# Kernel tuning notes

Hardware: AMD Instinct MI355X
Metric: run time of the kernel (lower is better)

Reference implementation:

```python
import jax, jax.numpy as jnp
import numpy as np

H, D = 16, 64  # num_attention_heads, attention_head_size
BASE = 10000.0

def _rope(q, k, seq_len):
    # RotaryPositionalEmbedding: inv_freq over arange(0, D, 2); emb = cat(freqs, freqs)
    inv_freq = 1.0 / (BASE ** (jnp.arange(0, D, 2, dtype=jnp.float32) / D))  # [D/2]=32
    pos = jnp.arange(seq_len, dtype=jnp.float32)
    freqs = jnp.outer(pos, inv_freq)            # [S, 32]; equals cos_emb[..., :d]
    cos, sin = jnp.cos(freqs), jnp.sin(freqs)   # [S, 32]
    d = D // 2                                   # 32: only first half of head dim rotated
    half = d // 2                                # 16: internal rotate-half within rot part
    def rot(x):  # x: [B, H, S, D]
        xr, xp = x[..., :d], x[..., d:]
        swapped = jnp.concatenate([xr[..., half:], xr[..., :half]], axis=-1)
        xr2 = xr * cos - swapped * sin
        return jnp.concatenate([xr2, xp], axis=-1)
    return rot(q), rot(k)

def setup_inputs() -> dict:
    key = jax.random.key(0)
    ks = jax.random.split(key, 9)
    B, S, E = 2, 2048, 1024
    std = 0.02  # initializer_range
    inp = {"hidden_states": jax.random.normal(ks[0], (B, S, E), jnp.float32)}
    for i, n in enumerate(["q", "k", "v", "d"]):
        inp[f"W{n}"] = jax.random.normal(ks[1 + 2 * i], (E, E), jnp.float32) * std
        inp[f"b{n}"] = jnp.zeros((E,), jnp.float32)
    return inp

def reference(hidden_states, Wq, bq, Wk, bk, Wv, bv, Wd, bd):
    B, S, E = hidden_states.shape
    def heads(x):  # [B,S,E] -> [B,H,S,D]
        return x.reshape(B, S, H, D).transpose(0, 2, 1, 3)
    q = heads(hidden_states @ Wq + bq)
    k = heads(hidden_states @ Wk + bk)
    v = heads(hidden_states @ Wv + bv)
    q, k = _rope(q, k, S)
    scores = jnp.einsum("bhqd,bhkd->bhqk", q, k) / jnp.sqrt(jnp.float32(D))
    causal = jnp.tril(jnp.ones((S, S), dtype=bool))
    scores = jnp.where(causal, scores, -jnp.inf)
    probs = jax.nn.softmax(scores, axis=-1)
    ctx = jnp.einsum("bhqk,bhkd->bhqd", probs, v)
    ctx = ctx.transpose(0, 2, 1, 3).reshape(B, S, E)
    return ctx @ Wd + bd
```

## Files before the change

kernel.cpp:

```cpp
#include <hip/hip_runtime.h>
#include <stdint.h>

typedef __bf16 bf8 __attribute__((ext_vector_type(8)));
typedef float f4 __attribute__((ext_vector_type(4)));
typedef float f16v __attribute__((ext_vector_type(16)));
typedef unsigned short us8 __attribute__((ext_vector_type(8)));
typedef unsigned short us4 __attribute__((ext_vector_type(4)));

#define MFMA16(a, b, c) __builtin_amdgcn_mfma_f32_16x16x32_bf16(a, b, c, 0, 0, 0)
#define MFMA32(a, b, c) __builtin_amdgcn_mfma_f32_32x32x16_bf16(a, b, c, 0, 0, 0)

__device__ __forceinline__ unsigned short f2b(float f) {
  union { float f; unsigned u; } x; x.f = f;
  unsigned u = x.u;
  u += 0x7fffu + ((u >> 16) & 1u);
  return (unsigned short)(u >> 16);
}

__device__ __forceinline__ unsigned cvtpk(float a, float b) {
  unsigned r;
  asm("v_cvt_pk_bf16_f32 %0, %1, %2" : "=v"(r) : "v"(a), "v"(b));
  return r;
}

__device__ __forceinline__ void plswap(unsigned &a, unsigned &b) {
  asm("v_permlane32_swap_b32 %0, %1" : "+v"(a), "+v"(b));
}

__device__ __forceinline__ void gload16(const void* g, void* l) {
  __builtin_amdgcn_global_load_lds(
      (const __attribute__((address_space(1))) void*)g,
      (__attribute__((address_space(3))) void*)l, 16, 0, 0);
}

__global__ __launch_bounds__(256) void prep_kernel(
    const float* __restrict__ W0, const float* __restrict__ W1,
    const float* __restrict__ W2, const float* __restrict__ W3,
    unsigned short* __restrict__ T0, unsigned short* __restrict__ T1,
    unsigned short* __restrict__ T2, unsigned short* __restrict__ T3,
    const float* __restrict__ hid, unsigned short* __restrict__ hb) {
  if (blockIdx.z == 4) {
    int bi = blockIdx.x + 32 * blockIdx.y;
#pragma unroll
    for (int k = 0; k < 4; ++k) {
      int i = bi * 1024 + k * 256 + threadIdx.x;
      float4 v = ((const float4*)hid)[i];
      us4 r = { f2b(v.x), f2b(v.y), f2b(v.z), f2b(v.w) };
      *(us4*)(hb + (size_t)i * 4) = r;
    }
    return;
  }
  const float* W; unsigned short* Wt;
  if (blockIdx.z == 0)      { W = W0; Wt = T0; }
  else if (blockIdx.z == 1) { W = W1; Wt = T1; }
  else if (blockIdx.z == 2) { W = W2; Wt = T2; }
  else                      { W = W3; Wt = T3; }
  __shared__ float tile[32][33];
  int tx = threadIdx.x & 31, ty = threadIdx.x >> 5;
  int kb = blockIdx.x * 32, nb = blockIdx.y * 32;
#pragma unroll
  for (int j = 0; j < 32; j += 8)
    tile[ty + j][tx] = W[(size_t)(kb + ty + j) * 1024 + nb + tx];
  __syncthreads();
#pragma unroll
  for (int j = 0; j < 32; j += 8)
    Wt[(size_t)(nb + ty + j) * 1024 + kb + tx] = f2b(tile[tx][ty + j]);
}

__global__ __launch_bounds__(256) void gemm_qkv_kernel(
    const unsigned short* __restrict__ X,
    const unsigned short* __restrict__ Wqt, const unsigned short* __restrict__ Wkt,
    const unsigned short* __restrict__ Wvt,
    const float* __restrict__ bq, const float* __restrict__ bk,
    const float* __restrict__ bv,
    unsigned short* __restrict__ Qo, unsigned short* __restrict__ Ko,
    unsigned short* __restrict__ Vo) {
  const unsigned short* Wt; const float* bias; unsigned short* out;
  if (blockIdx.z == 0)      { Wt = Wqt; bias = bq; out = Qo; }
  else if (blockIdx.z == 1) { Wt = Wkt; bias = bk; out = Ko; }
  else                      { Wt = Wvt; bias = bv; out = Vo; }

  __shared__ __align__(16) unsigned short shmem[128 * 136];
  unsigned short* As = shmem;
  unsigned short* Bs = shmem + 128 * 64;
  const int t = threadIdx.x;
  const int wave = t >> 6, lane = t & 63, quad = lane >> 4, l16 = lane & 15;
  const int wm = (wave >> 1) * 64, wn = (wave & 1) * 64;
  const int L = blockIdx.x + 8 * blockIdx.y;
  const int xcd = L & 7, w = L >> 3;
  const int m0 = (xcd * 4 + (w >> 3)) * 128;
  const int n0 = (w & 7) * 128;

  f4 acc[4][4];
#pragma unroll
  for (int mi = 0; mi < 4; ++mi)
#pragma unroll
    for (int ni = 0; ni < 4; ++ni) acc[mi][ni] = (f4)0.0f;

  for (int k0 = 0; k0 < 1024; k0 += 64) {
    __syncthreads();
#pragma unroll
    for (int it = 0; it < 4; ++it) {
      int chunk = it * 256 + wave * 64 + lane;
      int row = chunk >> 3, cc = chunk & 7;
      int csw = cc ^ (row & 7);
      gload16(&X[(size_t)(m0 + row) * 1024 + k0 + csw * 8],
              &As[(size_t)(it * 256 + wave * 64) * 8]);
      gload16(&Wt[(size_t)(n0 + row) * 1024 + k0 + csw * 8],
              &Bs[(size_t)(it * 256 + wave * 64) * 8]);
    }
    __syncthreads();
#pragma unroll
    for (int kk = 0; kk < 2; ++kk) {
      const int sw = (kk * 4 + quad) ^ (l16 & 7);
      bf8 a[4], b[4];
#pragma unroll
      for (int mi = 0; mi < 4; ++mi)
        a[mi] = *(const bf8*)&As[(wm + mi * 16 + l16) * 64 + sw * 8];
#pragma unroll
      for (int ni = 0; ni < 4; ++ni)
        b[ni] = *(const bf8*)&Bs[(wn + ni * 16 + l16) * 64 + sw * 8];
#pragma unroll
      for (int mi = 0; mi < 4; ++mi)
#pragma unroll
        for (int ni = 0; ni < 4; ++ni)
          acc[mi][ni] = MFMA16(a[mi], b[ni], acc[mi][ni]);
    }
  }

  float biasv[4];
#pragma unroll
  for (int ni = 0; ni < 4; ++ni) biasv[ni] = bias[n0 + wn + ni * 16 + l16];

  if (blockIdx.z < 2) {
    const float kr = 13.287712379549449f / 32.0f;
    const float f0 = exp2f(-(float)l16 * kr);
    const float f1 = exp2f(-(float)(l16 + 16) * kr);
    const float qs = (blockIdx.z == 0) ? 0.18033688011112042f : 1.0f;
#pragma unroll
    for (int mi = 0; mi < 4; ++mi) {
#pragma unroll
      for (int r = 0; r < 4; ++r) {
        int m = m0 + wm + mi * 16 + quad * 4 + r;
        float s = (float)(m & 2047);
        float s0, c0, s1, c1;
        __sincosf(s * f0, &s0, &c0);
        __sincosf(s * f1, &s1, &c1);
        float v0 = acc[mi][0][r] + biasv[0];
        float v1 = acc[mi][1][r] + biasv[1];
        acc[mi][0][r] = (v0 * c0 - v1 * s0) * qs;
        acc[mi][1][r] = (v1 * c1 - v0 * s1) * qs;
        acc[mi][2][r] = (acc[mi][2][r] + biasv[2]) * qs;
        acc[mi][3][r] = (acc[mi][3][r] + biasv[3]) * qs;
      }
    }
    __syncthreads();
#pragma unroll
    for (int ni = 0; ni < 4; ++ni)
#pragma unroll
      for (int mi = 0; mi < 4; ++mi)
#pragma unroll
        for (int r = 0; r < 4; ++r)
          shmem[(wm + mi * 16 + quad * 4 + r) * 136 + wn + ni * 16 + l16] =
              f2b(acc[mi][ni][r]);
    __syncthreads();
    const int b_ = m0 >> 11;
    const int sBase = m0 & 2047;
    if (blockIdx.z == 0) {
#pragma unroll
      for (int it = 0; it < 8; ++it) {
        int p = wave * 8 + it;
        int s3 = p >> 1, hloc = p & 1;
        int row = s3 * 8 + (lane >> 3);
        us8 v = *(const us8*)&shmem[row * 136 + hloc * 64 + (lane & 7) * 8];
        int h = (n0 >> 6) + hloc;
        *(us8*)&out[((size_t)(((b_ << 4) | h) * 2048 + sBase + row)) * 64 +
                    (lane & 7) * 8] = v;
      }
    } else {
#pragma unroll
      for (int it = 0; it < 8; ++it) {
        int p = wave * 8 + it;
        int s5 = p >> 3, hloc = (p >> 2) & 1, c4 = p & 3;
        int row = s5 * 32 + (lane & 31);
        int hl_ = lane >> 5;
        us8 v = *(const us8*)&shmem[row * 136 + hloc * 64 + c4 * 16 + hl_ * 8];
        int h = (n0 >> 6) + hloc;
        size_t off = (size_t)((b_ << 4) | h) * 131072
                   + (size_t)((sBase >> 5) + s5) * 2048 + (lane & 31) * 8
                   + c4 * 512 + hl_ * 256;
        *(us8*)&out[off] = v;
      }
    }
  } else {
#pragma unroll
    for (int ni = 0; ni < 4; ++ni) {
      int n = n0 + wn + ni * 16 + l16;
      int h = n >> 6, d = n & 63;
      int dpart = ((d >> 5) & 1) * 2048 + (d & 31) * 8;
#pragma unroll
      for (int mi = 0; mi < 4; ++mi) {
        int m = m0 + wm + mi * 16 + quad * 4;
        int b_ = m >> 11, s = m & 2047;
        us4 w2 = { f2b(acc[mi][ni][0] + biasv[ni]), f2b(acc[mi][ni][1] + biasv[ni]),
                   f2b(acc[mi][ni][2] + biasv[ni]), f2b(acc[mi][ni][3] + biasv[ni]) };
        size_t off = (size_t)((b_ << 4) | h) * 131072
                   + (size_t)(s >> 6) * 4096 + ((s >> 4) & 3) * 512
                   + ((s >> 3) & 1) * 256 + dpart + (s & 7);
        *(us4*)&out[off] = w2;
      }
    }
  }
}

__global__ __launch_bounds__(256) void flash_attn_kernel(
    const unsigned short* __restrict__ Q, const unsigned short* __restrict__ K,
    const unsigned short* __restrict__ Vt, unsigned short* __restrict__ ctx) {
  __shared__ __align__(16) float osh[2][64][36];
  __shared__ float lsh[2][64];
  const int t = threadIdx.x;
  const int lane = t & 63;
  const int wave = t >> 6, l32 = lane & 31, hl = lane >> 5;
  const int sub = wave >> 1;
  const int kh  = wave & 1;

  const int id = blockIdx.x;
  const int bh = id & 31;
  const int j = id >> 5;
  const int qt = (j & 16) ? (31 - (j & 15)) : (j & 15);
  const int b = bh >> 4, h = bh & 15;

  const unsigned short* Qh = Q + (size_t)bh * 131072;
  const unsigned short* Kh = K + (size_t)bh * 131072;
  const unsigned short* Vh = Vt + (size_t)bh * 131072;

  const int wrow0 = qt * 64 + sub * 32;
  const int q = wrow0 + l32;

  bf8 qb[4];
#pragma unroll
  for (int c = 0; c < 4; ++c)
    qb[c] = *(const bf8*)&Qh[(size_t)q * 64 + c * 16 + hl * 8];

  f16v o0 = (f16v)0.0f, o1 = (f16v)0.0f;
  float sum = 0.0f;

  bf8 kfA[2][4], kfB[2][4];
  const int nk = qt + 1;
  const int kb = kh ? (nk >> 1) : 0;
  const int ke = kh ? nk : (nk >> 1);

  auto loadK = [&](bf8 (&kf)[2][4], int kt) {
    const unsigned short* p = Kh + (size_t)kt * 4096 + lane * 8;
#pragma unroll
    for (int mt = 0; mt < 2; ++mt)
#pragma unroll
      for (int c = 0; c < 4; ++c)
        kf[mt][c] = *(const bf8*)&p[mt * 2048 + c * 512];
  };

  auto step = [&](int kt, bf8 (&kf)[2][4]) {
    const int k0 = kt * 64;

    f16v s0 = (f16v)0.0f, s1 = (f16v)0.0f;
#pragma unroll
    for (int c = 0; c < 4; ++c) {
      s0 = MFMA32(kf[0][c], qb[c], s0);
      s1 = MFMA32(kf[1][c], qb[c], s1);
    }
    __builtin_amdgcn_sched_barrier(0);

    const unsigned short* pv = Vh + (size_t)kt * 4096 + lane * 8;
    bf8 vf[2][4];
#pragma unroll
    for (int c = 0; c < 4; ++c)
#pragma unroll
      for (int dt = 0; dt < 2; ++dt)
        vf[dt][c] = *(const bf8*)&pv[dt * 2048 + c * 512];

    if (kt == nk - 1) {
#pragma unroll
      for (int gg = 0; gg < 4; ++gg)
#pragma unroll
        for (int i = 0; i < 4; ++i) {
          int kk = k0 + gg * 8 + hl * 4 + i;
          if (kk > q) s0[gg * 4 + i] = -3e38f;
          if (kk + 32 > q) s1[gg * 4 + i] = -3e38f;
        }
    }

    {
      uint2 pd2[4];
#pragma unroll
      for (int gg = 0; gg < 4; ++gg) {
        float p0 = exp2f(s0[gg * 4 + 0]), p1 = exp2f(s0[gg * 4 + 1]);
        float p2 = exp2f(s0[gg * 4 + 2]), p3 = exp2f(s0[gg * 4 + 3]);
        sum += (p0 + p1) + (p2 + p3);
        pd2[gg].x = cvtpk(p0, p1); pd2[gg].y = cvtpk(p2, p3);
      }
#pragma unroll
      for (int c = 0; c < 2; ++c) {
        unsigned ax = pd2[2 * c].x, bx = pd2[2 * c + 1].x;
        unsigned ay = pd2[2 * c].y, by = pd2[2 * c + 1].y;
        plswap(ax, bx);
        plswap(ay, by);
        union { uint4 u; bf8 v; } pv2; pv2.u = (uint4){ax, ay, bx, by};
        o0 = MFMA32(vf[0][c], pv2.v, o0);
        o1 = MFMA32(vf[1][c], pv2.v, o1);
      }
    }
    {
      uint2 pd2[4];
#pragma unroll
      for (int gg = 0; gg < 4; ++gg) {
        float r0 = exp2f(s1[gg * 4 + 0]), r1 = exp2f(s1[gg * 4 + 1]);
        float r2 = exp2f(s1[gg * 4 + 2]), r3 = exp2f(s1[gg * 4 + 3]);
        sum += (r0 + r1) + (r2 + r3);
        pd2[gg].x = cvtpk(r0, r1); pd2[gg].y = cvtpk(r2, r3);
      }
#pragma unroll
      for (int c = 0; c < 2; ++c) {
        unsigned ax = pd2[2 * c].x, bx = pd2[2 * c + 1].x;
        unsigned ay = pd2[2 * c].y, by = pd2[2 * c + 1].y;
        plswap(ax, bx);
        plswap(ay, by);
        union { uint4 u; bf8 v; } pv2; pv2.u = (uint4){ax, ay, bx, by};
        o0 = MFMA32(vf[0][2 + c], pv2.v, o0);
        o1 = MFMA32(vf[1][2 + c], pv2.v, o1);
      }
    }
  };

  if (kb < ke) {
    loadK(kfA, kb);
    int kt = kb;
    while (true) {
      if (kt + 1 < ke) loadK(kfB, kt + 1);
      step(kt, kfA);
      ++kt; if (kt >= ke) break;
      if (kt + 1 < ke) loadK(kfA, kt + 1);
      step(kt, kfB);
      ++kt; if (kt >= ke) break;
    }
  }

  float lpart = sum + __shfl_xor(sum, 32);

  if (kh == 0) {
#pragma unroll
    for (int gg = 0; gg < 4; ++gg) {
      f4 w0 = { o0[gg * 4 + 0], o0[gg * 4 + 1], o0[gg * 4 + 2], o0[gg * 4 + 3] };
      *(f4*)&osh[sub][lane][gg * 4] = w0;
      f4 w1 = { o1[gg * 4 + 0], o1[gg * 4 + 1], o1[gg * 4 + 2], o1[gg * 4 + 3] };
      *(f4*)&osh[sub][lane][16 + gg * 4] = w1;
    }
    lsh[sub][lane] = lpart;
  }
  __syncthreads();
  if (kh == 1) {
    float inv = 1.0f / (lpart + lsh[sub][lane]);
#pragma unroll
    for (int gg = 0; gg < 4; ++gg) {
      int d0 = gg * 8 + hl * 4;
      f4 a0 = *(f4*)&osh[sub][lane][gg * 4];
      f4 a1 = *(f4*)&osh[sub][lane][16 + gg * 4];
      us4 w0 = { f2b((o0[gg * 4 + 0] + a0[0]) * inv), f2b((o0[gg * 4 + 1] + a0[1]) * inv),
                 f2b((o0[gg * 4 + 2] + a0[2]) * inv), f2b((o0[gg * 4 + 3] + a0[3]) * inv) };
      *(us4*)&ctx[((size_t)(b * 2048 + q)) * 1024 + h * 64 + d0] = w0;
      us4 w1 = { f2b((o1[gg * 4 + 0] + a1[0]) * inv), f2b((o1[gg * 4 + 1] + a1[1]) * inv),
                 f2b((o1[gg * 4 + 2] + a1[2]) * inv), f2b((o1[gg * 4 + 3] + a1[3]) * inv) };
      *(us4*)&ctx[((size_t)(b * 2048 + q)) * 1024 + h * 64 + 32 + d0] = w1;
    }
  }
}

__global__ __launch_bounds__(256) void gemm_out_kernel(
    const unsigned short* __restrict__ A,
    const unsigned short* __restrict__ Wt,
    const float* __restrict__ bias, float* __restrict__ out) {
  __shared__ unsigned short As[64 * 64];
  __shared__ unsigned short Bs[128 * 64];
  const int t = threadIdx.x;
  const int wave = t >> 6, lane = t & 63, quad = lane >> 4, l16 = lane & 15;
  const int wm = (wave & 1) * 32, wn = (wave >> 1) * 64;
  const int L = blockIdx.x + 8 * blockIdx.y;
  const int xcd = L & 7, w = L >> 3;
  const int m0 = (xcd * 8 + (w >> 3)) * 64;
  const int n0 = (w & 7) * 128;

  f4 acc[2][4];
#pragma unroll
  for (int mi = 0; mi < 2; ++mi)
#pragma unroll
    for (int ni = 0; ni < 4; ++ni) acc[mi][ni] = (f4)0.0f;

  for (int k0 = 0; k0 < 1024; k0 += 64) {
    __syncthreads();
    {
#pragma unroll
      for (int it = 0; it < 2; ++it) {
        int chunk = it * 256 + wave * 64 + lane;
        int row = chunk >> 3, cc = chunk & 7;
        gload16(&A[(size_t)(m0 + row) * 1024 + k0 + (cc ^ (row & 7)) * 8],
                &As[(size_t)(it * 256 + wave * 64) * 8]);
      }
#pragma unroll
      for (int it = 0; it < 4; ++it) {
        int chunk = it * 256 + wave * 64 + lane;
        int row = chunk >> 3, cc = chunk & 7;
        gload16(&Wt[(size_t)(n0 + row) * 1024 + k0 + (cc ^ (row & 7)) * 8],
                &Bs[(size_t)(it * 256 + wave * 64) * 8]);
      }
    }
    __syncthreads();
#pragma unroll
    for (int kk = 0; kk < 2; ++kk) {
      const int sw = (kk * 4 + quad) ^ (l16 & 7);
      bf8 a[2], b[4];
#pragma unroll
      for (int mi = 0; mi < 2; ++mi)
        a[mi] = *(const bf8*)&As[(wm + mi * 16 + l16) * 64 + sw * 8];
#pragma unroll
      for (int ni = 0; ni < 4; ++ni)
        b[ni] = *(const bf8*)&Bs[(wn + ni * 16 + l16) * 64 + sw * 8];
#pragma unroll
      for (int mi = 0; mi < 2; ++mi)
#pragma unroll
        for (int ni = 0; ni < 4; ++ni)
          acc[mi][ni] = MFMA16(a[mi], b[ni], acc[mi][ni]);
    }
  }
#pragma unroll
  for (int ni = 0; ni < 4; ++ni) {
    int n = n0 + wn + ni * 16 + l16;
    float bv_ = bias[n];
#pragma unroll
    for (int mi = 0; mi < 2; ++mi) {
#pragma unroll
      for (int r = 0; r < 4; ++r) {
        int m = m0 + wm + mi * 16 + quad * 4 + r;
        out[(size_t)m * 1024 + n] = acc[mi][ni][r] + bv_;
      }
    }
  }
}

extern "C" void kernel_launch(void* const* d_in, const int* in_sizes, int n_in,
                              void* d_out, int out_size, void* d_ws, size_t ws_size,
                              hipStream_t stream) {
  const float* hidden = (const float*)d_in[0];
  const float* Wq = (const float*)d_in[1];
  const float* bq = (const float*)d_in[2];
  const float* Wk = (const float*)d_in[3];
  const float* bk = (const float*)d_in[4];
  const float* Wv = (const float*)d_in[5];
  const float* bv = (const float*)d_in[6];
  const float* Wd = (const float*)d_in[7];
  const float* bd = (const float*)d_in[8];
  float* out = (float*)d_out;

  char* ws = (char*)d_ws;
  unsigned short* Xb  = (unsigned short*)(ws);
  unsigned short* Wqt = (unsigned short*)(ws + ( 8ull << 20));
  unsigned short* Wkt = (unsigned short*)(ws + (10ull << 20));
  unsigned short* Wvt = (unsigned short*)(ws + (12ull << 20));
  unsigned short* Wdt = (unsigned short*)(ws + (14ull << 20));
  unsigned short* Qb  = (unsigned short*)(ws + (16ull << 20));
  unsigned short* Kb  = (unsigned short*)(ws + (24ull << 20));
  unsigned short* Vb  = (unsigned short*)(ws + (32ull << 20));
  unsigned short* Cb  = (unsigned short*)(ws + (40ull << 20));

  prep_kernel<<<dim3(32, 32, 5), 256, 0, stream>>>(
      Wq, Wk, Wv, Wd, Wqt, Wkt, Wvt, Wdt, hidden, Xb);
  gemm_qkv_kernel<<<dim3(8, 32, 3), 256, 0, stream>>>(
      Xb, Wqt, Wkt, Wvt, bq, bk, bv, Qb, Kb, Vb);
  flash_attn_kernel<<<1024, 256, 0, stream>>>(Qb, Kb, Vb, Cb);
  gemm_out_kernel<<<dim3(8, 64), 256, 0, stream>>>(Cb, Wdt, bd, out);
}
```

Before: 193.6 us.

## Stage K/V tiles in LDS shared by four waves over 128-row query tiles

The attention kernel now gives each block 128 query rows, one 32-row slice per wave, instead of 64 rows split across two key halves. K and V tiles are loaded once per block into double-buffered shared memory with async global-to-LDS loads, so all four waves reuse them rather than each wave reading from global memory. The shared-memory split-K reduction of partial outputs is removed, and the grid is halved. The cost is two barriers per key tile, and waves whose rows end before the diagonal sit idle on later tiles.

After: 197.1 us. No clear change (+1.8%).

```diff
diff --git a/kernel.cpp b/kernel.cpp
--- a/kernel.cpp
+++ b/kernel.cpp
@@ -216,26 +216,24 @@
 __global__ __launch_bounds__(256) void flash_attn_kernel(
     const unsigned short* __restrict__ Q, const unsigned short* __restrict__ K,
     const unsigned short* __restrict__ Vt, unsigned short* __restrict__ ctx) {
-  __shared__ __align__(16) float osh[2][64][36];
-  __shared__ float lsh[2][64];
+  __shared__ __align__(16) unsigned short Ks[2][4096];
+  __shared__ __align__(16) unsigned short Vs[2][4096];
   const int t = threadIdx.x;
   const int lane = t & 63;
   const int wave = t >> 6, l32 = lane & 31, hl = lane >> 5;
-  const int sub = wave >> 1;
-  const int kh  = wave & 1;
 
   const int id = blockIdx.x;
   const int bh = id & 31;
   const int j = id >> 5;
-  const int qt = (j & 16) ? (31 - (j & 15)) : (j & 15);
+  const int qt = (j < 8) ? (15 - j) : (j - 8);
   const int b = bh >> 4, h = bh & 15;
 
   const unsigned short* Qh = Q + (size_t)bh * 131072;
   const unsigned short* Kh = K + (size_t)bh * 131072;
   const unsigned short* Vh = Vt + (size_t)bh * 131072;
 
-  const int wrow0 = qt * 64 + sub * 32;
-  const int q = wrow0 + l32;
+  const int r0 = qt * 128 + wave * 32;
+  const int q = r0 + l32;
 
   bf8 qb[4];
 #pragma unroll
@@ -245,22 +243,28 @@
   f16v o0 = (f16v)0.0f, o1 = (f16v)0.0f;
   float sum = 0.0f;
 
-  bf8 kfA[2][4], kfB[2][4];
-  const int nk = qt + 1;
-  const int kb = kh ? (nk >> 1) : 0;
-  const int ke = kh ? nk : (nk >> 1);
-
-  auto loadK = [&](bf8 (&kf)[2][4], int kt) {
-    const unsigned short* p = Kh + (size_t)kt * 4096 + lane * 8;
+  const int nk = 2 * qt + 2;
+
+  auto stage = [&](int buf, int kt) {
+    const unsigned short* gK = Kh + (size_t)kt * 4096;
+    const unsigned short* gV = Vh + (size_t)kt * 4096;
+#pragma unroll
+    for (int it = 0; it < 2; ++it) {
+      int base = it * 256 + wave * 64;
+      gload16(gK + (size_t)(base + lane) * 8, &Ks[buf][base * 8]);
+      gload16(gV + (size_t)(base + lane) * 8, &Vs[buf][base * 8]);
+    }
+  };
+
+  auto step = [&](int kt, int cur) {
+    const int k0 = kt * 64;
+    const unsigned short* kp = &Ks[cur][lane * 8];
+    bf8 kf[2][4];
 #pragma unroll
     for (int mt = 0; mt < 2; ++mt)
 #pragma unroll
       for (int c = 0; c < 4; ++c)
-        kf[mt][c] = *(const bf8*)&p[mt * 2048 + c * 512];
-  };
-
-  auto step = [&](int kt, bf8 (&kf)[2][4]) {
-    const int k0 = kt * 64;
+        kf[mt][c] = *(const bf8*)&kp[mt * 2048 + c * 512];
 
     f16v s0 = (f16v)0.0f, s1 = (f16v)0.0f;
 #pragma unroll
@@ -270,15 +274,15 @@
     }
     __builtin_amdgcn_sched_barrier(0);
 
-    const unsigned short* pv = Vh + (size_t)kt * 4096 + lane * 8;
+    const unsigned short* vp = &Vs[cur][lane * 8];
     bf8 vf[2][4];
 #pragma unroll
     for (int c = 0; c < 4; ++c)
 #pragma unroll
       for (int dt = 0; dt < 2; ++dt)
-        vf[dt][c] = *(const bf8*)&pv[dt * 2048 + c * 512];
-
-    if (kt == nk - 1) {
+        vf[dt][c] = *(const bf8*)&vp[dt * 2048 + c * 512];
+
+    if (k0 + 63 > r0) {
 #pragma unroll
       for (int gg = 0; gg < 4; ++gg)
 #pragma unroll
@@ -313,10 +317,10 @@
       uint2 pd2[4];
 #pragma unroll
       for (int gg = 0; gg < 4; ++gg) {
-        float r0 = exp2f(s1[gg * 4 + 0]), r1 = exp2f(s1[gg * 4 + 1]);
-        float r2 = exp2f(s1[gg * 4 + 2]), r3 = exp2f(s1[gg * 4 + 3]);
-        sum += (r0 + r1) + (r2 + r3);
-        pd2[gg].x = cvtpk(r0, r1); pd2[gg].y = cvtpk(r2, r3);
+        float r0f = exp2f(s1[gg * 4 + 0]), r1f = exp2f(s1[gg * 4 + 1]);
+        float r2f = exp2f(s1[gg * 4 + 2]), r3f = exp2f(s1[gg * 4 + 3]);
+        sum += (r0f + r1f) + (r2f + r3f);
+        pd2[gg].x = cvtpk(r0f, r1f); pd2[gg].y = cvtpk(r2f, r3f);
       }
 #pragma unroll
       for (int c = 0; c < 2; ++c) {
@@ -331,46 +335,35 @@
     }
   };
 
-  if (kb < ke) {
-    loadK(kfA, kb);
-    int kt = kb;
-    while (true) {
-      if (kt + 1 < ke) loadK(kfB, kt + 1);
-      step(kt, kfA);
-      ++kt; if (kt >= ke) break;
-      if (kt + 1 < ke) loadK(kfA, kt + 1);
-      step(kt, kfB);
-      ++kt; if (kt >= ke) break;
-    }
-  }
-
-  float lpart = sum + __shfl_xor(sum, 32);
-
-  if (kh == 0) {
-#pragma unroll
-    for (int gg = 0; gg < 4; ++gg) {
-      f4 w0 = { o0[gg * 4 + 0], o0[gg * 4 + 1], o0[gg * 4 + 2], o0[gg * 4 + 3] };
-      *(f4*)&osh[sub][lane][gg * 4] = w0;
-      f4 w1 = { o1[gg * 4 + 0], o1[gg * 4 + 1], o1[gg * 4 + 2], o1[gg * 4 + 3] };
-      *(f4*)&osh[sub][lane][16 + gg * 4] = w1;
-    }
-    lsh[sub][lane] = lpart;
-  }
-  __syncthreads();
-  if (kh == 1) {
-    float inv = 1.0f / (lpart + lsh[sub][lane]);
-#pragma unroll
-    for (int gg = 0; gg < 4; ++gg) {
-      int d0 = gg * 8 + hl * 4;
-      f4 a0 = *(f4*)&osh[sub][lane][gg * 4];
-      f4 a1 = *(f4*)&osh[sub][lane][16 + gg * 4];
-      us4 w0 = { f2b((o0[gg * 4 + 0] + a0[0]) * inv), f2b((o0[gg * 4 + 1] + a0[1]) * inv),
-                 f2b((o0[gg * 4 + 2] + a0[2]) * inv), f2b((o0[gg * 4 + 3] + a0[3]) * inv) };
-      *(us4*)&ctx[((size_t)(b * 2048 + q)) * 1024 + h * 64 + d0] = w0;
-      us4 w1 = { f2b((o1[gg * 4 + 0] + a1[0]) * inv), f2b((o1[gg * 4 + 1] + a1[1]) * inv),
-                 f2b((o1[gg * 4 + 2] + a1[2]) * inv), f2b((o1[gg * 4 + 3] + a1[3]) * inv) };
-      *(us4*)&ctx[((size_t)(b * 2048 + q)) * 1024 + h * 64 + 32 + d0] = w1;
-    }
+  stage(0, 0);
+  for (int kt = 0; kt < nk; ++kt) {
+    const int cur = kt & 1;
+    if (kt + 1 < nk) {
+      stage(cur ^ 1, kt + 1);
+      asm volatile("s_waitcnt vmcnt(4)" ::: "memory");
+    } else {
+      asm volatile("s_waitcnt vmcnt(0)" ::: "memory");
+    }
+    __builtin_amdgcn_s_barrier();
+    __builtin_amdgcn_sched_barrier(0);
+    if (kt * 64 <= r0 + 31)
+      step(kt, cur);
+    asm volatile("s_waitcnt lgkmcnt(0)" ::: "memory");
+    __builtin_amdgcn_s_barrier();
+    __builtin_amdgcn_sched_barrier(0);
+  }
+
+  float lrow = sum + __shfl_xor(sum, 32);
+  float inv = 1.0f / lrow;
+#pragma unroll
+  for (int gg = 0; gg < 4; ++gg) {
+    int d0 = gg * 8 + hl * 4;
+    us4 w0 = { f2b(o0[gg * 4 + 0] * inv), f2b(o0[gg * 4 + 1] * inv),
+               f2b(o0[gg * 4 + 2] * inv), f2b(o0[gg * 4 + 3] * inv) };
+    *(us4*)&ctx[((size_t)(b * 2048 + q)) * 1024 + h * 64 + d0] = w0;
+    us4 w1 = { f2b(o1[gg * 4 + 0] * inv), f2b(o1[gg * 4 + 1] * inv),
+               f2b(o1[gg * 4 + 2] * inv), f2b(o1[gg * 4 + 3] * inv) };
+    *(us4*)&ctx[((size_t)(b * 2048 + q)) * 1024 + h * 64 + 32 + d0] = w1;
   }
 }
 
@@ -474,6 +467,6 @@
       Wq, Wk, Wv, Wd, Wqt, Wkt, Wvt, Wdt, hidden, Xb);
   gemm_qkv_kernel<<<dim3(8, 32, 3), 256, 0, stream>>>(
       Xb, Wqt, Wkt, Wvt, bq, bk, bv, Qb, Kb, Vb);
-  flash_attn_kernel<<<1024, 256, 0, stream>>>(Qb, Kb, Vb, Cb);
+  flash_attn_kernel<<<512, 256, 0, stream>>>(Qb, Kb, Vb, Cb);
   gemm_out_kernel<<<dim3(8, 64), 256, 0, stream>>>(Cb, Wdt, bd, out);
 }
```
